# Kernel optimization log

Measured on AMD Instinct MI355X. Metric: run time of the kernel, lower is better.

## Reference

```python
import jax, jax.numpy as jnp
import numpy as np

EMB = 1024

def setup_inputs() -> dict:
    key = jax.random.key(0)
    ks = jax.random.split(key, 6)
    T, k1, k2, D = 64, 256, 1024, EMB
    scale = 1.0 / np.sqrt(D)
    return {
        "fast_feature": jax.random.normal(ks[0], (T, k2, D), jnp.float32),
        "slow_feature": jax.random.normal(ks[1], (T, k1, D), jnp.float32),
        "fast_W": jax.random.normal(ks[2], (D, D), jnp.float32) * scale,
        "fast_b": jax.random.normal(ks[3], (D,), jnp.float32) * 0.01,
        "slow_W": jax.random.normal(ks[4], (D, D), jnp.float32) * scale,
        "slow_b": jax.random.normal(ks[5], (D,), jnp.float32) * 0.01,
    }

def reference(fast_feature, slow_feature, fast_W, fast_b, slow_W, slow_b):
    # Linear projections (torch Linear: x @ W.T + b)
    fast_key = jnp.einsum('tkd,ed->tke', fast_feature, fast_W) + fast_b  # [T,k2,D]
    slow_key = jnp.einsum('tkd,ed->tke', slow_feature, slow_W) + slow_b  # [T,k1,D]
    # Scaled dot-product similarity fast->slow
    sim = jnp.einsum('tqd,tkd->tqk', fast_key, slow_key)  # [T,k2,k1]
    sim = sim / jnp.sqrt(jnp.asarray(slow_feature.shape[-1], sim.dtype))
    attn = jax.nn.softmax(sim, axis=-1)
    ctx = jnp.einsum('tqk,tkd->tqd', attn, slow_feature)  # note: values are raw slow_feature
    return fast_feature + ctx
```

## Files before the change

### kernel.cpp

```cpp
#include <hip/hip_runtime.h>
#include <stdint.h>

typedef __attribute__((ext_vector_type(8))) short bf16x8;
typedef __attribute__((ext_vector_type(4))) float f32x4;

__device__ __forceinline__ unsigned short f2bf(float f) {
  unsigned int u = __builtin_bit_cast(unsigned int, f);
  u += 0x7FFFu + ((u >> 16) & 1u);
  return (unsigned short)(u >> 16);
}

__device__ __forceinline__ float bf2f(unsigned short s) {
  return __builtin_bit_cast(float, (unsigned int)s << 16);
}

__device__ __forceinline__ void gload_lds16(const void* g, void* l) {
  __builtin_amdgcn_global_load_lds(
      (__attribute__((address_space(1))) void*)(uintptr_t)g,
      (__attribute__((address_space(3))) void*)l,
      16, 0, 0);
}

#define BARRIER() do { asm volatile("" ::: "memory"); __builtin_amdgcn_s_barrier(); asm volatile("" ::: "memory"); } while (0)
#define WAITVM(N) asm volatile("s_waitcnt vmcnt(" #N ")" ::: "memory")

template <int MODE>
__global__ __launch_bounds__(512, 2) void gemm8(
    const unsigned short* __restrict__ A, const unsigned short* __restrict__ B,
    void* __restrict__ Cv, const void* __restrict__ aux, int N, int K,
    int nm, int nn, long sAB, long sBB, long sCB, long sXB, float scale)
{
  __shared__ __align__(16) char lds[131072];
  char* ldsc = lds;

  const int tid = threadIdx.x;
  const int lane = tid & 63;
  const int wid = tid >> 6;
  const int fr = lane & 15, fq = lane >> 4;

  const int nwg = gridDim.x;
  const int id = blockIdx.x;
  const int swz = (id & 7) * (nwg >> 3) + (id >> 3);
  const int per = nm * nn;
  const int t = swz / per;
  const int rem = swz - t * per;
  const int mi_ = rem / nn, ni_ = rem - mi_ * nn;
  const long bm = (long)mi_ * 256, bn = (long)ni_ * 256;

  const unsigned short* Ag = A + (long)t * sAB + bm * K;
  const unsigned short* Bg = B + (long)t * sBB + bn * K;
  const int NT = K >> 6;

  const unsigned short* aS[2][2];
  const unsigned short* bS[2][2];
#pragma unroll
  for (int p = 0; p < 2; ++p) {
    const int q = p * 512 + tid;
    const int lr = q >> 3, cs = q & 7;
    const int cl = cs ^ (lr & 7);
#pragma unroll
    for (int h = 0; h < 2; ++h) {
      const int gA = ((lr >> 6) << 7) | (h << 6) | (lr & 63);
      const int gB = ((lr >> 5) << 6) | (h << 5) | (lr & 31);
      aS[p][h] = Ag + (long)gA * K + cl * 8;
      bS[p][h] = Bg + (long)gB * K + cl * 8;
    }
  }

  const int c0 = ((fq ^ (fr & 3)) + ((fr >> 2) & 1) * 4) * 16;
  const int aRd = ((wid >> 2) * 64 + fr) * 128 + c0;
  const int bRd = ((wid & 3) * 32 + fr) * 128 + c0;

  f32x4 acc[2][2][4][2];
#pragma unroll
  for (int a = 0; a < 2; a++)
#pragma unroll
    for (int b = 0; b < 2; b++)
#pragma unroll
      for (int i = 0; i < 4; i++)
#pragma unroll
        for (int j = 0; j < 2; j++)
#pragma unroll
          for (int r = 0; r < 4; r++) acc[a][b][i][j][r] = 0.f;

  bf16x8 af[4][2], bf[2][2][2];

#define STAGE(srcArr, aoff, h, ktv, b) do {                                   \
  _Pragma("unroll")                                                           \
  for (int p = 0; p < 2; ++p)                                                 \
    gload_lds16(srcArr[p][h] + ((long)(ktv) << 6),                            \
                ldsc + (aoff) + ((b) << 16) + ((h) << 14) + (p << 13) + (wid << 10)); \
} while (0)

#define LDA(mi, cub) do {                                                     \
  _Pragma("unroll")                                                           \
  for (int i = 0; i < 4; ++i) {                                               \
    af[i][0] = *(const bf16x8*)(ldsc + (cub) + (mi) * 16384 + aRd + i * 2048);        \
    af[i][1] = *(const bf16x8*)(ldsc + (cub) + (mi) * 16384 + (aRd ^ 64) + i * 2048); \
  }                                                                           \
} while (0)

#define LDB(nj, cub) do {                                                     \
  _Pragma("unroll")                                                           \
  for (int j = 0; j < 2; ++j) {                                               \
    bf[nj][j][0] = *(const bf16x8*)(ldsc + 32768 + (cub) + (nj) * 16384 + bRd + j * 2048);        \
    bf[nj][j][1] = *(const bf16x8*)(ldsc + 32768 + (cub) + (nj) * 16384 + (bRd ^ 64) + j * 2048); \
  }                                                                           \
} while (0)

#define QUAD(mi, nj) do {                                                     \
  __builtin_amdgcn_s_setprio(1);                                              \
  _Pragma("unroll")                                                           \
  for (int i = 0; i < 4; ++i)                                                 \
  _Pragma("unroll")                                                           \
  for (int j = 0; j < 2; ++j) {                                               \
    acc[mi][nj][i][j] = __builtin_amdgcn_mfma_f32_16x16x32_bf16(              \
        af[i][0], bf[nj][j][0], acc[mi][nj][i][j], 0, 0, 0);                  \
    acc[mi][nj][i][j] = __builtin_amdgcn_mfma_f32_16x16x32_bf16(              \
        af[i][1], bf[nj][j][1], acc[mi][nj][i][j], 0, 0, 0);                  \
  }                                                                           \
  __builtin_amdgcn_s_setprio(0);                                              \
} while (0)

  STAGE(aS, 0, 0, 0, 0);
  STAGE(bS, 32768, 0, 0, 0);
  STAGE(bS, 32768, 1, 0, 0);
  STAGE(aS, 0, 1, 0, 0);
  if (NT > 1) {
    STAGE(aS, 0, 0, 1, 1);
    STAGE(bS, 32768, 0, 1, 1);
    STAGE(bS, 32768, 1, 1, 1);
    WAITVM(6);
  } else {
    WAITVM(0);
  }
  BARRIER();

  for (int kt = 0; kt < NT; ++kt) {
    const int cur = kt & 1, nxt = cur ^ 1;
    const int cub = cur << 16;
    LDA(0, cub);
    LDB(0, cub);
    if (kt + 1 < NT) STAGE(aS, 0, 1, kt + 1, nxt);
    BARRIER();
    QUAD(0, 0);
    BARRIER();
    LDB(1, cub);
    if (kt + 2 < NT) STAGE(aS, 0, 0, kt + 2, cur);
    BARRIER();
    QUAD(0, 1);
    BARRIER();
    LDA(1, cub);
    if (kt + 2 < NT) STAGE(bS, 32768, 0, kt + 2, cur);
    BARRIER();
    QUAD(1, 0);
    BARRIER();
    if (kt + 2 < NT) {
      STAGE(bS, 32768, 1, kt + 2, cur);
      QUAD(1, 1);
      WAITVM(6);
    } else {
      QUAD(1, 1);
      WAITVM(0);
    }
    BARRIER();
  }

  if (MODE == 1) {
    float* red  = (float*)ldsc;
    float* red2 = (float*)(ldsc + 4096);
    const int wc = wid & 3;
    const int rbase = (wid >> 2) * 128;
#pragma unroll
    for (int mi = 0; mi < 2; ++mi)
#pragma unroll
      for (int i = 0; i < 4; ++i)
#pragma unroll
        for (int r = 0; r < 4; ++r) {
          float m = fmaxf(fmaxf(acc[mi][0][i][0][r], acc[mi][0][i][1][r]),
                          fmaxf(acc[mi][1][i][0][r], acc[mi][1][i][1][r]));
#pragma unroll
          for (int o = 1; o <= 8; o <<= 1) m = fmaxf(m, __shfl_xor(m, o));
          if (fr == 0) red[(rbase + mi * 64 + i * 16 + fq * 4 + r) * 4 + wc] = m;
        }
    BARRIER();
#pragma unroll
    for (int mi = 0; mi < 2; ++mi)
#pragma unroll
      for (int i = 0; i < 4; ++i)
#pragma unroll
        for (int r = 0; r < 4; ++r) {
          const int rl = rbase + mi * 64 + i * 16 + fq * 4 + r;
          f32x4 mm = *(f32x4*)&red[rl * 4];
          const float M = fmaxf(fmaxf(mm[0], mm[1]), fmaxf(mm[2], mm[3]));
          float s = 0.f;
#pragma unroll
          for (int nj = 0; nj < 2; ++nj)
#pragma unroll
            for (int j = 0; j < 2; ++j) {
              float e = __expf((acc[mi][nj][i][j][r] - M) * scale);
              acc[mi][nj][i][j][r] = e;
              s += e;
            }
#pragma unroll
          for (int o = 1; o <= 8; o <<= 1) s += __shfl_xor(s, o);
          if (fr == 0) red2[rl * 4 + wc] = s;
        }
    BARRIER();
    unsigned short* C = (unsigned short*)Cv + (long)t * sCB;
#pragma unroll
    for (int mi = 0; mi < 2; ++mi)
#pragma unroll
      for (int i = 0; i < 4; ++i)
#pragma unroll
        for (int r = 0; r < 4; ++r) {
          const int rl = rbase + mi * 64 + i * 16 + fq * 4 + r;
          f32x4 sv = *(f32x4*)&red2[rl * 4];
          const float inv = 1.0f / (sv[0] + sv[1] + sv[2] + sv[3]);
          const long gr = bm + rl;
#pragma unroll
          for (int nj = 0; nj < 2; ++nj)
#pragma unroll
            for (int j = 0; j < 2; ++j) {
              const long gcol = bn + wc * 64 + nj * 32 + j * 16 + fr;
              C[gr * N + gcol] = f2bf(acc[mi][nj][i][j][r] * inv);
            }
        }
  } else {
#pragma unroll
    for (int mi = 0; mi < 2; ++mi)
#pragma unroll
      for (int nj = 0; nj < 2; ++nj)
#pragma unroll
        for (int i = 0; i < 4; ++i) {
          const long grow0 = bm + (wid >> 2) * 128 + mi * 64 + i * 16 + fq * 4;
#pragma unroll
          for (int j = 0; j < 2; ++j) {
            const long gcol = bn + (wid & 3) * 64 + nj * 32 + j * 16 + fr;
            if (MODE == 0) {
              unsigned short* C = (unsigned short*)Cv + (long)t * sCB;
              const float bv = ((const float*)aux)[gcol];
#pragma unroll
              for (int r = 0; r < 4; ++r)
                C[(grow0 + r) * N + gcol] = f2bf(acc[mi][nj][i][j][r] + bv);
            } else {
              float* C = (float*)Cv + (long)t * sCB;
              const unsigned short* X = (const unsigned short*)aux + (long)t * sXB;
#pragma unroll
              for (int r = 0; r < 4; ++r) {
                const long idx = (grow0 + r) * N + gcol;
                C[idx] = acc[mi][nj][i][j][r] + bf2f(X[idx]);
              }
            }
          }
        }
  }
#undef STAGE
#undef LDA
#undef LDB
#undef QUAD
}

__global__ __launch_bounds__(256) void convert_f32_bf16(
    const float* __restrict__ in, unsigned short* __restrict__ out, long n) {
  long i = ((long)blockIdx.x * 256 + threadIdx.x) * 4;
  long stride = (long)gridDim.x * 1024;
  for (; i < n; i += stride) {
    float4 v = *(const float4*)(in + i);
    ushort4 o;
    o.x = f2bf(v.x); o.y = f2bf(v.y); o.z = f2bf(v.z); o.w = f2bf(v.w);
    *(ushort4*)(out + i) = o;
  }
}

__global__ __launch_bounds__(256) void convert_transpose_slow(
    const float* __restrict__ in, unsigned short* __restrict__ outR,
    unsigned short* __restrict__ outT) {
  __shared__ unsigned short tile[32][33];
  int t = blockIdx.z;
  int d0 = blockIdx.x * 32;
  int k0 = blockIdx.y * 32;
  const float* ip = in + (long)t * 256 * 1024;
  unsigned short* rp = outR + (long)t * 256 * 1024;
  unsigned short* tp = outT + (long)t * 1024 * 256;
  int tx = threadIdx.x & 31, ty = threadIdx.x >> 5;
#pragma unroll
  for (int p = 0; p < 4; p++) {
    int k = ty + p * 8;
    unsigned short b = f2bf(ip[(long)(k0 + k) * 1024 + d0 + tx]);
    tile[k][tx] = b;
    rp[(long)(k0 + k) * 1024 + d0 + tx] = b;
  }
  __syncthreads();
#pragma unroll
  for (int p = 0; p < 4; p++) {
    int d = ty + p * 8;
    tp[(long)(d0 + d) * 256 + k0 + tx] = tile[tx][d];
  }
}

extern "C" void kernel_launch(void* const* d_in, const int* in_sizes, int n_in,
                              void* d_out, int out_size, void* d_ws, size_t ws_size,
                              hipStream_t stream) {
  const float* fastF     = (const float*)d_in[0];
  const float* slowF     = (const float*)d_in[1];
  const float* fastW     = (const float*)d_in[2];
  const float* fast_bias = (const float*)d_in[3];
  const float* slowW     = (const float*)d_in[4];
  const float* slow_bias = (const float*)d_in[5];
  float* out = (float*)d_out;

  char* ws = (char*)d_ws;
  unsigned short* fastBf  = (unsigned short*)(ws);
  unsigned short* fastKey = (unsigned short*)(ws + 134217728L);
  unsigned short* slowBf  = (unsigned short*)(ws + 268435456L);
  unsigned short* attnBf  = (unsigned short*)(ws + 268435456L);
  unsigned short* slowT   = (unsigned short*)(ws + 301989888L);
  unsigned short* slowKey = (unsigned short*)(ws + 335544320L);
  unsigned short* fWb     = (unsigned short*)(ws + 369098752L);
  unsigned short* sWb     = (unsigned short*)(ws + 371195904L);

  convert_f32_bf16<<<2048, 256, 0, stream>>>(fastF, fastBf, 67108864L);
  convert_f32_bf16<<<1024, 256, 0, stream>>>(fastW, fWb, 1048576L);
  convert_f32_bf16<<<1024, 256, 0, stream>>>(slowW, sWb, 1048576L);
  convert_transpose_slow<<<dim3(32, 8, 64), 256, 0, stream>>>(slowF, slowBf, slowT);

  gemm8<0><<<64 * 4, 512, 0, stream>>>(slowBf, sWb, slowKey, slow_bias,
      1024, 1024, 64, 4, 0, 0, 0, 0, 1.f);
  gemm8<0><<<256 * 4, 512, 0, stream>>>(fastBf, fWb, fastKey, fast_bias,
      1024, 1024, 256, 4, 0, 0, 0, 0, 1.f);
  gemm8<1><<<4 * 1 * 64, 512, 0, stream>>>(fastKey, slowKey, attnBf, nullptr,
      256, 1024, 4, 1, 1048576L, 262144L, 262144L, 0, 0.03125f);
  gemm8<2><<<4 * 4 * 64, 512, 0, stream>>>(attnBf, slowT, out, fastBf,
      1024, 256, 4, 4, 262144L, 262144L, 1048576L, 1048576L, 1.f);
}
```

Measured before the change: 469.8 us.

## Add 128x128-tile GEMM kernel for projections and output, keep 256-tile softmax GEMM

Adds a gemm4 kernel that uses 128x128 output tiles, 64 KB of LDS and launch bounds allowing four blocks per CU. It replaces the 256x256-tile kernel for the two linear projections and the attention-times-values output GEMM. The softmax GEMM stays on the large-tile kernel, now split out as gemm8_sm. Smaller tiles give more blocks and more occupancy to hide latency, at the cost of lower operand reuse per tile and more global/LDS traffic.

```diff
diff --git a/kernel.cpp b/kernel.cpp
--- a/kernel.cpp
+++ b/kernel.cpp
@@ -25,10 +25,169 @@
 #define WAITVM(N) asm volatile("s_waitcnt vmcnt(" #N ")" ::: "memory")
 
 template <int MODE>
-__global__ __launch_bounds__(512, 2) void gemm8(
+__global__ __launch_bounds__(512, 4) void gemm4(
     const unsigned short* __restrict__ A, const unsigned short* __restrict__ B,
     void* __restrict__ Cv, const void* __restrict__ aux, int N, int K,
     int nm, int nn, long sAB, long sBB, long sCB, long sXB, float scale)
+{
+  __shared__ __align__(16) char lds[65536];
+  char* ldsc = lds;
+
+  const int tid = threadIdx.x;
+  const int lane = tid & 63;
+  const int wid = tid >> 6;
+  const int fr = lane & 15, fq = lane >> 4;
+
+  const int nwg = gridDim.x;
+  const int id = blockIdx.x;
+  const int swz = (id & 7) * (nwg >> 3) + (id >> 3);
+  const int per = nm * nn;
+  const int t = swz / per;
+  const int rem = swz - t * per;
+  const int mi_ = rem / nn, ni_ = rem - mi_ * nn;
+  const long bm = (long)mi_ * 128, bn = (long)ni_ * 128;
+
+  const unsigned short* Ag = A + (long)t * sAB + bm * K;
+  const unsigned short* Bg = B + (long)t * sBB + bn * K;
+  const int NT = K >> 6;
+
+  const unsigned short* aS[2];
+  const unsigned short* bS[2];
+  {
+    const int lr = tid >> 3, cs = tid & 7;
+    const int cl = cs ^ (lr & 7);
+#pragma unroll
+    for (int h = 0; h < 2; ++h) {
+      const int gA = ((lr >> 5) << 6) | (h << 5) | (lr & 31);
+      const int gB = ((lr >> 4) << 5) | (h << 4) | (lr & 15);
+      aS[h] = Ag + (long)gA * K + cl * 8;
+      bS[h] = Bg + (long)gB * K + cl * 8;
+    }
+  }
+
+  const int c0 = ((fq ^ (fr & 3)) + ((fr >> 2) & 1) * 4) * 16;
+  const int aRd = ((wid >> 2) * 32 + fr) * 128 + c0;
+  const int bRd = ((wid & 3) * 16 + fr) * 128 + c0;
+
+  f32x4 acc[2][2][2];
+#pragma unroll
+  for (int a = 0; a < 2; a++)
+#pragma unroll
+    for (int b = 0; b < 2; b++)
+#pragma unroll
+      for (int i = 0; i < 2; i++)
+#pragma unroll
+        for (int r = 0; r < 4; r++) acc[a][b][i][r] = 0.f;
+
+  bf16x8 af[2][2], bf[2][2];
+
+#define STAGE(srcArr, aoff, h, ktv, b)                                        \
+  gload_lds16(srcArr[h] + ((long)(ktv) << 6),                                 \
+              ldsc + (aoff) + ((b) << 14) + ((h) << 13) + (wid << 10))
+
+#define LDA(mi, cub) do {                                                     \
+  _Pragma("unroll")                                                           \
+  for (int i = 0; i < 2; ++i) {                                               \
+    af[i][0] = *(const bf16x8*)(ldsc + (cub) + (mi) * 8192 + aRd + i * 2048);        \
+    af[i][1] = *(const bf16x8*)(ldsc + (cub) + (mi) * 8192 + (aRd ^ 64) + i * 2048); \
+  }                                                                           \
+} while (0)
+
+#define LDB(nj, cub) do {                                                     \
+  bf[nj][0] = *(const bf16x8*)(ldsc + 32768 + (cub) + (nj) * 8192 + bRd);        \
+  bf[nj][1] = *(const bf16x8*)(ldsc + 32768 + (cub) + (nj) * 8192 + (bRd ^ 64)); \
+} while (0)
+
+#define QUAD(mi, nj) do {                                                     \
+  __builtin_amdgcn_s_setprio(1);                                              \
+  _Pragma("unroll")                                                           \
+  for (int i = 0; i < 2; ++i) {                                               \
+    acc[mi][nj][i] = __builtin_amdgcn_mfma_f32_16x16x32_bf16(                 \
+        af[i][0], bf[nj][0], acc[mi][nj][i], 0, 0, 0);                        \
+    acc[mi][nj][i] = __builtin_amdgcn_mfma_f32_16x16x32_bf16(                 \
+        af[i][1], bf[nj][1], acc[mi][nj][i], 0, 0, 0);                        \
+  }                                                                           \
+  __builtin_amdgcn_s_setprio(0);                                              \
+} while (0)
+
+  STAGE(aS, 0, 0, 0, 0);
+  STAGE(bS, 32768, 0, 0, 0);
+  STAGE(bS, 32768, 1, 0, 0);
+  STAGE(aS, 0, 1, 0, 0);
+  if (NT > 1) {
+    STAGE(aS, 0, 0, 1, 1);
+    STAGE(bS, 32768, 0, 1, 1);
+    STAGE(bS, 32768, 1, 1, 1);
+    WAITVM(3);
+  } else {
+    WAITVM(0);
+  }
+  BARRIER();
+
+  for (int kt = 0; kt < NT; ++kt) {
+    const int cur = kt & 1, nxt = cur ^ 1;
+    const int cub = cur << 14;
+    LDA(0, cub);
+    LDB(0, cub);
+    if (kt + 1 < NT) STAGE(aS, 0, 1, kt + 1, nxt);
+    BARRIER();
+    QUAD(0, 0);
+    BARRIER();
+    LDB(1, cub);
+    if (kt + 2 < NT) STAGE(aS, 0, 0, kt + 2, cur);
+    BARRIER();
+    QUAD(0, 1);
+    BARRIER();
+    LDA(1, cub);
+    if (kt + 2 < NT) STAGE(bS, 32768, 0, kt + 2, cur);
+    BARRIER();
+    QUAD(1, 0);
+    BARRIER();
+    if (kt + 2 < NT) {
+      STAGE(bS, 32768, 1, kt + 2, cur);
+      QUAD(1, 1);
+      WAITVM(3);
+    } else {
+      QUAD(1, 1);
+      WAITVM(0);
+    }
+    BARRIER();
+  }
+
+#pragma unroll
+  for (int mi = 0; mi < 2; ++mi)
+#pragma unroll
+    for (int nj = 0; nj < 2; ++nj)
+#pragma unroll
+      for (int i = 0; i < 2; ++i) {
+        const long grow0 = bm + (wid >> 2) * 64 + mi * 32 + i * 16 + fq * 4;
+        const long gcol = bn + (wid & 3) * 32 + nj * 16 + fr;
+        if (MODE == 0) {
+          unsigned short* C = (unsigned short*)Cv + (long)t * sCB;
+          const float bv = ((const float*)aux)[gcol];
+#pragma unroll
+          for (int r = 0; r < 4; ++r)
+            C[(grow0 + r) * N + gcol] = f2bf(acc[mi][nj][i][r] + bv);
+        } else {
+          float* C = (float*)Cv + (long)t * sCB;
+          const unsigned short* X = (const unsigned short*)aux + (long)t * sXB;
+#pragma unroll
+          for (int r = 0; r < 4; ++r) {
+            const long idx = (grow0 + r) * N + gcol;
+            C[idx] = acc[mi][nj][i][r] + bf2f(X[idx]);
+          }
+        }
+      }
+#undef STAGE
+#undef LDA
+#undef LDB
+#undef QUAD
+}
+
+__global__ __launch_bounds__(512, 2) void gemm8_sm(
+    const unsigned short* __restrict__ A, const unsigned short* __restrict__ B,
+    unsigned short* __restrict__ Cv, int N, int K,
+    int nm, int nn, long sAB, long sBB, long sCB, float scale)
 {
   __shared__ __align__(16) char lds[131072];
   char* ldsc = lds;
@@ -166,7 +325,7 @@
     BARRIER();
   }
 
-  if (MODE == 1) {
+  {
     float* red  = (float*)ldsc;
     float* red2 = (float*)(ldsc + 4096);
     const int wc = wid & 3;
@@ -207,7 +366,7 @@
           if (fr == 0) red2[rl * 4 + wc] = s;
         }
     BARRIER();
-    unsigned short* C = (unsigned short*)Cv + (long)t * sCB;
+    unsigned short* C = Cv + (long)t * sCB;
 #pragma unroll
     for (int mi = 0; mi < 2; ++mi)
 #pragma unroll
@@ -225,34 +384,6 @@
               const long gcol = bn + wc * 64 + nj * 32 + j * 16 + fr;
               C[gr * N + gcol] = f2bf(acc[mi][nj][i][j][r] * inv);
             }
-        }
-  } else {
-#pragma unroll
-    for (int mi = 0; mi < 2; ++mi)
-#pragma unroll
-      for (int nj = 0; nj < 2; ++nj)
-#pragma unroll
-        for (int i = 0; i < 4; ++i) {
-          const long grow0 = bm + (wid >> 2) * 128 + mi * 64 + i * 16 + fq * 4;
-#pragma unroll
-          for (int j = 0; j < 2; ++j) {
-            const long gcol = bn + (wid & 3) * 64 + nj * 32 + j * 16 + fr;
-            if (MODE == 0) {
-              unsigned short* C = (unsigned short*)Cv + (long)t * sCB;
-              const float bv = ((const float*)aux)[gcol];
-#pragma unroll
-              for (int r = 0; r < 4; ++r)
-                C[(grow0 + r) * N + gcol] = f2bf(acc[mi][nj][i][j][r] + bv);
-            } else {
-              float* C = (float*)Cv + (long)t * sCB;
-              const unsigned short* X = (const unsigned short*)aux + (long)t * sXB;
-#pragma unroll
-              for (int r = 0; r < 4; ++r) {
-                const long idx = (grow0 + r) * N + gcol;
-                C[idx] = acc[mi][nj][i][j][r] + bf2f(X[idx]);
-              }
-            }
-          }
         }
   }
 #undef STAGE
@@ -325,12 +456,12 @@
   convert_f32_bf16<<<1024, 256, 0, stream>>>(slowW, sWb, 1048576L);
   convert_transpose_slow<<<dim3(32, 8, 64), 256, 0, stream>>>(slowF, slowBf, slowT);
 
-  gemm8<0><<<64 * 4, 512, 0, stream>>>(slowBf, sWb, slowKey, slow_bias,
-      1024, 1024, 64, 4, 0, 0, 0, 0, 1.f);
-  gemm8<0><<<256 * 4, 512, 0, stream>>>(fastBf, fWb, fastKey, fast_bias,
-      1024, 1024, 256, 4, 0, 0, 0, 0, 1.f);
-  gemm8<1><<<4 * 1 * 64, 512, 0, stream>>>(fastKey, slowKey, attnBf, nullptr,
-      256, 1024, 4, 1, 1048576L, 262144L, 262144L, 0, 0.03125f);
-  gemm8<2><<<4 * 4 * 64, 512, 0, stream>>>(attnBf, slowT, out, fastBf,
-      1024, 256, 4, 4, 262144L, 262144L, 1048576L, 1048576L, 1.f);
-}
+  gemm4<0><<<128 * 8, 512, 0, stream>>>(slowBf, sWb, slowKey, slow_bias,
+      1024, 1024, 128, 8, 0, 0, 0, 0, 1.f);
+  gemm4<0><<<512 * 8, 512, 0, stream>>>(fastBf, fWb, fastKey, fast_bias,
+      1024, 1024, 512, 8, 0, 0, 0, 0, 1.f);
+  gemm8_sm<<<4 * 1 * 64, 512, 0, stream>>>(fastKey, slowKey, attnBf,
+      256, 1024, 4, 1, 1048576L, 262144L, 262144L, 0.03125f);
+  gemm4<2><<<8 * 8 * 64, 512, 0, stream>>>(attnBf, slowT, out, fastBf,
+      1024, 256, 8, 8, 262144L, 262144L, 1048576L, 1048576L, 1.f);
+}
```

Result: slower. 510.1 us (+8.6%).
